# Kernel tuning notes

Hardware: AMD Instinct MI355X
Metric: run time of the kernel (lower is better)

## Reference

```python
import jax, jax.numpy as jnp
import numpy as np

R = 16  # number of attention heads


def setup_inputs() -> dict:
    key = jax.random.key(0)
    ks = jax.random.split(key, 6)
    B, T, D = 2, 2048, 1024
    s = 1.0 / np.sqrt(D)
    return {
        "q": jax.random.normal(ks[0], (B, T, D), jnp.float32),
        "k": jax.random.normal(ks[1], (B, T, D), jnp.float32),
        "q_map": jax.random.normal(ks[2], (D, D), jnp.float32) * s,
        "k_map": jax.random.normal(ks[3], (D, D), jnp.float32) * s,
        "v_map": jax.random.normal(ks[4], (D, D), jnp.float32) * s,
        "output_map": jax.random.normal(ks[5], (D, D), jnp.float32) * s,
    }


def _split_heads(x, r):
    # [B, T, D] -> [B, r, T, D//r]
    B, T, D = x.shape
    return x.reshape(B, T, r, D // r).transpose(0, 2, 1, 3)


def reference(q, k, q_map, k_map, v_map, output_map):
    # v = k (the layer reuses Keys as Values)
    B, Tq, D = q.shape
    dh = D // R
    qh = _split_heads(q @ q_map, R)  # [B, r, Tq, dh]
    kh = _split_heads(k @ k_map, R)  # [B, r, Tk, dh]
    vh = _split_heads(k @ v_map, R)  # [B, r, Tk, dh]
    scale = 1.0 / jnp.sqrt(jnp.asarray(dh, qh.dtype))
    scores = jnp.einsum('brqd,brkd->brqk', qh, kh) * scale
    weights = jax.nn.softmax(scores, axis=-1)  # dropout=0 / inference -> identity
    out = jnp.einsum('brqk,brkd->brqd', weights, vh)  # [B, r, Tq, dh]
    merged = out.transpose(0, 2, 1, 3).reshape(B, Tq, D)
    return merged @ output_map
```

## Files before the change

### kernel.cpp

```cpp
#include <hip/hip_runtime.h>
#include <hip/hip_bf16.h>


typedef unsigned short u16;
typedef __attribute__((ext_vector_type(8))) short short8;
typedef __attribute__((ext_vector_type(4))) float f32x4;

__device__ __forceinline__ u16 f2bf(float f) {
  __hip_bfloat16 h = __float2bfloat16(f);
  return reinterpret_cast<u16&>(h);
}

__device__ __forceinline__ void gl_lds16(const u16* g, u16* l) {
  __builtin_amdgcn_global_load_lds(
      (const __attribute__((address_space(1))) void*)g,
      (__attribute__((address_space(3))) void*)l, 16, 0, 0);
}

template <int ROWS>
__device__ __forceinline__ void stage_tile(const u16* __restrict__ g, int gs,
                                           u16* lds, int wave, int lane) {
  const int lr8 = lane >> 3;
  const int gc = ((lane & 7) ^ lr8) * 8;
#pragma unroll
  for (int w = 0; w < ROWS / 32; ++w) {
    int t = w * 4 + wave;
    gl_lds16(g + (size_t)(t * 8 + lr8) * gs + gc, lds + t * 512);
  }
}

__global__ __launch_bounds__(256)
void convert_qk(const float4* __restrict__ q, const float4* __restrict__ k,
                u16* __restrict__ qb, u16* __restrict__ kb) {
  int i = blockIdx.x * 256 + threadIdx.x;
  float4 qv = q[i], kv = k[i];
  ushort4 qo, ko;
  qo.x = f2bf(qv.x); qo.y = f2bf(qv.y); qo.z = f2bf(qv.z); qo.w = f2bf(qv.w);
  ko.x = f2bf(kv.x); ko.y = f2bf(kv.y); ko.z = f2bf(kv.z); ko.w = f2bf(kv.w);
  reinterpret_cast<ushort4*>(qb)[i] = qo;
  reinterpret_cast<ushort4*>(kb)[i] = ko;
}

__global__ __launch_bounds__(256)
void convert_maps(const float* __restrict__ qm, const float* __restrict__ km,
                  const float* __restrict__ vm, const float* __restrict__ om,
                  u16* __restrict__ qmT, u16* __restrict__ kmT,
                  u16* __restrict__ vmT, u16* __restrict__ omT) {
  __shared__ float t[32][33];
  const float* src; u16* dst; float scale = 1.0f;
  switch (blockIdx.z) {
    case 0:  src = qm; dst = qmT; scale = 0.125f; break;
    case 1:  src = km; dst = kmT; break;
    case 2:  src = vm; dst = vmT; break;
    default: src = om; dst = omT; break;
  }
  int nb0 = blockIdx.x * 32, kb0 = blockIdx.y * 32;
  int c = threadIdx.x & 31, rq = threadIdx.x >> 5;
#pragma unroll
  for (int j = 0; j < 4; ++j)
    t[rq * 4 + j][c] = src[(size_t)(kb0 + rq * 4 + j) * 1024 + nb0 + c];
  __syncthreads();
#pragma unroll
  for (int j = 0; j < 4; ++j) {
    int nn = rq * 4 + j;
    dst[(size_t)(nb0 + nn) * 1024 + kb0 + c] = f2bf(t[c][nn] * scale);
  }
}

__global__ __launch_bounds__(256)
void gemm_qkv(const u16* __restrict__ qb, const u16* __restrict__ kb,
              const u16* __restrict__ Bt, u16* __restrict__ Qp,
              u16* __restrict__ Kp, u16* __restrict__ Vt) {
  __shared__ u16 As[2][128 * 64];
  __shared__ u16 Bs[2][128 * 64];
  const int tid = threadIdx.x;
  const int wave = tid >> 6, lane = tid & 63;
  const int lr = lane & 15, lg = lane >> 4;
  const int xx = blockIdx.x;
  const int m0 = blockIdx.y * 128, n0 = xx * 128;
  const int wm = (wave >> 1) * 64, wn = (wave & 1) * 64;
  const u16* A = (xx < 8) ? qb : kb;

  f32x4 acc[4][4] = {};
  const int K = 1024;
  const u16* Ab = A + (size_t)m0 * K;
  const u16* Bb = Bt + (size_t)n0 * K;

  stage_tile<128>(Ab, K, &As[0][0], wave, lane);
  stage_tile<128>(Bb, K, &Bs[0][0], wave, lane);
  __syncthreads();

  int cur = 0;
  for (int kt = 0; kt < 16; ++kt) {
    if (kt + 1 < 16) {
      stage_tile<128>(Ab + (kt + 1) * 64, K, &As[cur ^ 1][0], wave, lane);
      stage_tile<128>(Bb + (kt + 1) * 64, K, &Bs[cur ^ 1][0], wave, lane);
    }
#pragma unroll
    for (int ks = 0; ks < 2; ++ks) {
      short8 af[4], bfr[4];
#pragma unroll
      for (int i = 0; i < 4; ++i) {
        int ar = wm + i * 16 + lr;
        int ac = (ks * 4 + lg) ^ (ar & 7);
        af[i] = *reinterpret_cast<const short8*>(&As[cur][ar * 64 + ac * 8]);
      }
#pragma unroll
      for (int j = 0; j < 4; ++j) {
        int br = wn + j * 16 + lr;
        int bc = (ks * 4 + lg) ^ (br & 7);
        bfr[j] = *reinterpret_cast<const short8*>(&Bs[cur][br * 64 + bc * 8]);
      }
#pragma unroll
      for (int i = 0; i < 4; ++i)
#pragma unroll
        for (int j = 0; j < 4; ++j)
          acc[i][j] = __builtin_amdgcn_mfma_f32_16x16x32_bf16(af[i], bfr[j], acc[i][j], 0, 0, 0);
    }
    __syncthreads();
    cur ^= 1;
  }

#pragma unroll
  for (int i = 0; i < 4; ++i) {
    int row0 = m0 + wm + i * 16 + lg * 4;
#pragma unroll
    for (int j = 0; j < 4; ++j) {
      int col = n0 + wn + j * 16 + lr;
      if (xx < 8) {
#pragma unroll
        for (int r = 0; r < 4; ++r)
          Qp[(size_t)(row0 + r) * 1024 + col] = f2bf(acc[i][j][r]);
      } else if (xx < 16) {
#pragma unroll
        for (int r = 0; r < 4; ++r)
          Kp[(size_t)(row0 + r) * 1024 + (col - 1024)] = f2bf(acc[i][j][r]);
      } else {
        int bb = row0 >> 11, kk = row0 & 2047;
        int hd = col - 2048;
        uint2 pk;
        pk.x = (unsigned)f2bf(acc[i][j][0]) | ((unsigned)f2bf(acc[i][j][1]) << 16);
        pk.y = (unsigned)f2bf(acc[i][j][2]) | ((unsigned)f2bf(acc[i][j][3]) << 16);
        *reinterpret_cast<uint2*>(&Vt[(size_t)(bb * 1024 + hd) * 2048 + kk]) = pk;
      }
    }
  }
}

__global__ __launch_bounds__(256)
void gemm_out(const u16* __restrict__ A, const u16* __restrict__ Bt,
              float* __restrict__ C, int K, int ldc) {
  __shared__ u16 As[2][128 * 64];
  __shared__ u16 Bs[2][64 * 64];
  const int tid = threadIdx.x;
  const int wave = tid >> 6, lane = tid & 63;
  const int lr = lane & 15, lg = lane >> 4;
  const int m0 = blockIdx.y * 128, n0 = blockIdx.x * 64;
  const int wm = (wave >> 1) * 64, wn = (wave & 1) * 32;

  f32x4 acc[4][2] = {};
  const int kT = K >> 6;
  const u16* Ab = A + (size_t)m0 * K;
  const u16* Bb = Bt + (size_t)n0 * K;

  stage_tile<128>(Ab, K, &As[0][0], wave, lane);
  stage_tile<64>(Bb, K, &Bs[0][0], wave, lane);
  __syncthreads();

  int cur = 0;
  for (int kt = 0; kt < kT; ++kt) {
    if (kt + 1 < kT) {
      stage_tile<128>(Ab + (kt + 1) * 64, K, &As[cur ^ 1][0], wave, lane);
      stage_tile<64>(Bb + (kt + 1) * 64, K, &Bs[cur ^ 1][0], wave, lane);
    }
#pragma unroll
    for (int ks = 0; ks < 2; ++ks) {
      short8 af[4], bfr[2];
#pragma unroll
      for (int i = 0; i < 4; ++i) {
        int ar = wm + i * 16 + lr;
        int ac = (ks * 4 + lg) ^ (ar & 7);
        af[i] = *reinterpret_cast<const short8*>(&As[cur][ar * 64 + ac * 8]);
      }
#pragma unroll
      for (int j = 0; j < 2; ++j) {
        int br = wn + j * 16 + lr;
        int bc = (ks * 4 + lg) ^ (br & 7);
        bfr[j] = *reinterpret_cast<const short8*>(&Bs[cur][br * 64 + bc * 8]);
      }
#pragma unroll
      for (int i = 0; i < 4; ++i)
#pragma unroll
        for (int j = 0; j < 2; ++j)
          acc[i][j] = __builtin_amdgcn_mfma_f32_16x16x32_bf16(af[i], bfr[j], acc[i][j], 0, 0, 0);
    }
    __syncthreads();
    cur ^= 1;
  }
#pragma unroll
  for (int i = 0; i < 4; ++i) {
    int row0 = m0 + wm + i * 16 + lg * 4;
#pragma unroll
    for (int j = 0; j < 2; ++j) {
      int col = n0 + wn + j * 16 + lr;
#pragma unroll
      for (int r = 0; r < 4; ++r)
        C[(size_t)(row0 + r) * ldc + col] = acc[i][j][r];
    }
  }
}

__global__ __launch_bounds__(256)
void attention(const u16* __restrict__ Qp, const u16* __restrict__ Kp,
               const u16* __restrict__ Vt, u16* __restrict__ merged) {
  __shared__ u16 Ks[2][64 * 64];
  __shared__ u16 Vs[2][64 * 64];
  __shared__ unsigned Pbuf[8][512];
  const int tid = threadIdx.x;
  const int wave = tid >> 6, lane = tid & 63;
  const int lr = lane & 15, lg = lane >> 4;
  const int qt = blockIdx.x, h = blockIdx.y, b = blockIdx.z;
  const int q0 = qt * 128;

  short8 qf[2][2];
#pragma unroll
  for (int qm = 0; qm < 2; ++qm) {
    const size_t qrow = (size_t)(b * 2048 + q0 + wave * 32 + qm * 16 + lr);
#pragma unroll
    for (int ks = 0; ks < 2; ++ks)
      qf[qm][ks] = *reinterpret_cast<const short8*>(
          &Qp[qrow * 1024 + h * 64 + ks * 32 + lg * 8]);
  }

  f32x4 oacc[2][4] = {};
  float ell[2] = {0.f, 0.f};

  const u16* Kg = Kp + (size_t)(b * 2048) * 1024 + h * 64;
  const u16* Vg = Vt + (size_t)(b * 1024 + h * 64) * 2048;

  stage_tile<64>(Kg, 1024, &Ks[0][0], wave, lane);
  stage_tile<64>(Vg, 2048, &Vs[0][0], wave, lane);
  __syncthreads();

  int cur = 0;
  for (int ktile = 0; ktile < 32; ++ktile) {
    if (ktile + 1 < 32) {
      const int kn = (ktile + 1) * 64;
      stage_tile<64>(Kg + (size_t)kn * 1024, 1024, &Ks[cur ^ 1][0], wave, lane);
      stage_tile<64>(Vg + kn, 2048, &Vs[cur ^ 1][0], wave, lane);
    }
    short8 kfr[4][2];
#pragma unroll
    for (int kf = 0; kf < 4; ++kf) {
      int br = kf * 16 + lr;
#pragma unroll
      for (int ks = 0; ks < 2; ++ks) {
        int bc = (ks * 4 + lg) ^ (br & 7);
        kfr[kf][ks] = *reinterpret_cast<const short8*>(&Ks[cur][br * 64 + bc * 8]);
      }
    }
#pragma unroll
    for (int qm = 0; qm < 2; ++qm) {
      unsigned* Pw = &Pbuf[wave * 2 + qm][0];
#pragma unroll
      for (int kf = 0; kf < 4; ++kf) {
        f32x4 z = {};
#pragma unroll
        for (int ks = 0; ks < 2; ++ks)
          z = __builtin_amdgcn_mfma_f32_16x16x32_bf16(kfr[kf][ks], qf[qm][ks], z, 0, 0, 0);
        float p0 = __expf(z[0]), p1 = __expf(z[1]);
        float p2 = __expf(z[2]), p3 = __expf(z[3]);
        ell[qm] += (p0 + p1) + (p2 + p3);
        uint2 pk;
        pk.x = (unsigned)f2bf(p0) | ((unsigned)f2bf(p1) << 16);
        pk.y = (unsigned)f2bf(p2) | ((unsigned)f2bf(p3) << 16);
        *reinterpret_cast<uint2*>(&Pw[((kf * 16 + lr) * 4 + lg) * 2]) = pk;
      }
    }
    asm volatile("s_waitcnt lgkmcnt(0)" ::: "memory");
    __builtin_amdgcn_sched_barrier(0);
#pragma unroll
    for (int ks = 0; ks < 2; ++ks) {
      short8 pa[2];
#pragma unroll
      for (int qm = 0; qm < 2; ++qm)
        pa[qm] = *reinterpret_cast<const short8*>(
            &Pbuf[wave * 2 + qm][(((ks * 2 + (lg >> 1)) * 16 + lr) * 4 + 2 * (lg & 1)) * 2]);
#pragma unroll
      for (int df = 0; df < 4; ++df) {
        int vr = df * 16 + lr;
        int vc = (ks * 4 + lg) ^ (vr & 7);
        short8 vb = *reinterpret_cast<const short8*>(&Vs[cur][vr * 64 + vc * 8]);
#pragma unroll
        for (int qm = 0; qm < 2; ++qm)
          oacc[qm][df] = __builtin_amdgcn_mfma_f32_16x16x32_bf16(pa[qm], vb, oacc[qm][df], 0, 0, 0);
      }
    }
    __syncthreads();
    cur ^= 1;
  }
#pragma unroll
  for (int qm = 0; qm < 2; ++qm) {
    float e = ell[qm];
    e += __shfl_xor(e, 16);
    e += __shfl_xor(e, 32);
    float inv = 1.0f / e;
    float invr[4];
#pragma unroll
    for (int r = 0; r < 4; ++r) invr[r] = __shfl(inv, lg * 4 + r);
    const size_t rowbase = (size_t)(b * 2048 + q0 + wave * 32 + qm * 16 + lg * 4);
#pragma unroll
    for (int df = 0; df < 4; ++df)
#pragma unroll
      for (int r = 0; r < 4; ++r)
        merged[(rowbase + r) * 1024 + h * 64 + df * 16 + lr] =
            f2bf(oacc[qm][df][r] * invr[r]);
  }
}

extern "C" void kernel_launch(void* const* d_in, const int* in_sizes, int n_in,
                              void* d_out, int out_size, void* d_ws, size_t ws_size,
                              hipStream_t stream) {
  const float* q  = (const float*)d_in[0];
  const float* k  = (const float*)d_in[1];
  const float* qm = (const float*)d_in[2];
  const float* km = (const float*)d_in[3];
  const float* vm = (const float*)d_in[4];
  const float* om = (const float*)d_in[5];
  float* out = (float*)d_out;

  char* w = (char*)d_ws;
  const size_t MB = 1024 * 1024;
  u16* qb  = (u16*)(w + 0 * MB);
  u16* kb  = (u16*)(w + 8 * MB);
  u16* qmT = (u16*)(w + 16 * MB);
  u16* kmT = (u16*)(w + 18 * MB);
  u16* vmT = (u16*)(w + 20 * MB);
  u16* omT = (u16*)(w + 22 * MB);
  u16* Qp  = (u16*)(w + 24 * MB);
  u16* Kp  = (u16*)(w + 32 * MB);
  u16* Vt  = (u16*)(w + 48 * MB);
  u16* merged = qb;

  convert_qk<<<4096, 256, 0, stream>>>((const float4*)q, (const float4*)k, qb, kb);
  convert_maps<<<dim3(32, 32, 4), 256, 0, stream>>>(qm, km, vm, om, qmT, kmT, vmT, omT);
  gemm_qkv<<<dim3(24, 32), 256, 0, stream>>>(qb, kb, qmT, Qp, Kp, Vt);
  attention<<<dim3(16, 16, 2), 256, 0, stream>>>(Qp, Kp, Vt, merged);
  gemm_out<<<dim3(16, 32), 256, 0, stream>>>(merged, omT, out, 1024, 1024);
}
```

Baseline: 229.3 us.

## Use exp2 with folded log2e, MFMA row sums, packed bf16 conversion

Folds log2(e) into the Q projection scale so the softmax can use the native exp2 instruction instead of __expf. The softmax denominator is now accumulated by an MFMA of the bf16 P tile against a vector of ones, replacing the per-lane scalar adds and the final cross-lane shuffles. The P buffer is relaid out as uint2 with packed two-wide bf16 conversions. The trade is an extra MFMA per P fragment in exchange for fewer VALU ops, and the denominator is now summed from bf16-rounded probabilities, which slightly changes rounding.

```diff
diff --git a/kernel.cpp b/kernel.cpp
--- a/kernel.cpp
+++ b/kernel.cpp
@@ -9,6 +9,11 @@
 __device__ __forceinline__ u16 f2bf(float f) {
   __hip_bfloat16 h = __float2bfloat16(f);
   return reinterpret_cast<u16&>(h);
+}
+
+__device__ __forceinline__ unsigned pack2bf(float a, float b) {
+  __hip_bfloat162 h2 = __float22bfloat162_rn(make_float2(a, b));
+  return reinterpret_cast<unsigned&>(h2);
 }
 
 __device__ __forceinline__ void gl_lds16(const u16* g, u16* l) {
@@ -49,7 +54,7 @@
   __shared__ float t[32][33];
   const float* src; u16* dst; float scale = 1.0f;
   switch (blockIdx.z) {
-    case 0:  src = qm; dst = qmT; scale = 0.125f; break;
+    case 0:  src = qm; dst = qmT; scale = 0.125f * 1.4426950408889634f; break;
     case 1:  src = km; dst = kmT; break;
     case 2:  src = vm; dst = vmT; break;
     default: src = om; dst = omT; break;
@@ -215,7 +220,7 @@
                const u16* __restrict__ Vt, u16* __restrict__ merged) {
   __shared__ u16 Ks[2][64 * 64];
   __shared__ u16 Vs[2][64 * 64];
-  __shared__ unsigned Pbuf[8][512];
+  __shared__ uint2 Pbuf[8][256];
   const int tid = threadIdx.x;
   const int wave = tid >> 6, lane = tid & 63;
   const int lr = lane & 15, lg = lane >> 4;
@@ -232,8 +237,12 @@
           &Qp[qrow * 1024 + h * 64 + ks * 32 + lg * 8]);
   }
 
+  short8 ones;
+#pragma unroll
+  for (int j = 0; j < 8; ++j) ones[j] = (short)0x3F80;
+
   f32x4 oacc[2][4] = {};
-  float ell[2] = {0.f, 0.f};
+  f32x4 lacc[2] = {};
 
   const u16* Kg = Kp + (size_t)(b * 2048) * 1024 + h * 64;
   const u16* Vg = Vt + (size_t)(b * 1024 + h * 64) * 2048;
@@ -261,20 +270,19 @@
     }
 #pragma unroll
     for (int qm = 0; qm < 2; ++qm) {
-      unsigned* Pw = &Pbuf[wave * 2 + qm][0];
+      uint2* Pq = &Pbuf[wave * 2 + qm][0];
 #pragma unroll
       for (int kf = 0; kf < 4; ++kf) {
         f32x4 z = {};
 #pragma unroll
         for (int ks = 0; ks < 2; ++ks)
           z = __builtin_amdgcn_mfma_f32_16x16x32_bf16(kfr[kf][ks], qf[qm][ks], z, 0, 0, 0);
-        float p0 = __expf(z[0]), p1 = __expf(z[1]);
-        float p2 = __expf(z[2]), p3 = __expf(z[3]);
-        ell[qm] += (p0 + p1) + (p2 + p3);
+        float p0 = __builtin_amdgcn_exp2f(z[0]), p1 = __builtin_amdgcn_exp2f(z[1]);
+        float p2 = __builtin_amdgcn_exp2f(z[2]), p3 = __builtin_amdgcn_exp2f(z[3]);
         uint2 pk;
-        pk.x = (unsigned)f2bf(p0) | ((unsigned)f2bf(p1) << 16);
-        pk.y = (unsigned)f2bf(p2) | ((unsigned)f2bf(p3) << 16);
-        *reinterpret_cast<uint2*>(&Pw[((kf * 16 + lr) * 4 + lg) * 2]) = pk;
+        pk.x = pack2bf(p0, p1);
+        pk.y = pack2bf(p2, p3);
+        Pq[(kf * 4 + lg) * 16 + lr] = pk;
       }
     }
     asm volatile("s_waitcnt lgkmcnt(0)" ::: "memory");
@@ -283,9 +291,16 @@
     for (int ks = 0; ks < 2; ++ks) {
       short8 pa[2];
 #pragma unroll
-      for (int qm = 0; qm < 2; ++qm)
-        pa[qm] = *reinterpret_cast<const short8*>(
-            &Pbuf[wave * 2 + qm][(((ks * 2 + (lg >> 1)) * 16 + lr) * 4 + 2 * (lg & 1)) * 2]);
+      for (int qm = 0; qm < 2; ++qm) {
+        const uint2* Pq = &Pbuf[wave * 2 + qm][0];
+        const int kfs = ks * 2 + (lg >> 1);
+        uint2 u0 = Pq[(kfs * 4 + 2 * (lg & 1) + 0) * 16 + lr];
+        uint2 u1 = Pq[(kfs * 4 + 2 * (lg & 1) + 1) * 16 + lr];
+        union { uint4 u; short8 s; } pu;
+        pu.u.x = u0.x; pu.u.y = u0.y; pu.u.z = u1.x; pu.u.w = u1.y;
+        pa[qm] = pu.s;
+        lacc[qm] = __builtin_amdgcn_mfma_f32_16x16x32_bf16(pa[qm], ones, lacc[qm], 0, 0, 0);
+      }
 #pragma unroll
       for (int df = 0; df < 4; ++df) {
         int vr = df * 16 + lr;
@@ -301,13 +316,9 @@
   }
 #pragma unroll
   for (int qm = 0; qm < 2; ++qm) {
-    float e = ell[qm];
-    e += __shfl_xor(e, 16);
-    e += __shfl_xor(e, 32);
-    float inv = 1.0f / e;
     float invr[4];
 #pragma unroll
-    for (int r = 0; r < 4; ++r) invr[r] = __shfl(inv, lg * 4 + r);
+    for (int r = 0; r < 4; ++r) invr[r] = 1.0f / lacc[qm][r];
     const size_t rowbase = (size_t)(b * 2048 + q0 + wave * 32 + qm * 16 + lg * 4);
 #pragma unroll
     for (int df = 0; df < 4; ++df)
```

After: 223.1 us. 2.7% less time.
